# Kernel tuning notes

Hardware: AMD Instinct MI355X
Metric: run time of the kernel (lower is better)

The kernel has to match this reference:

```python
import jax, jax.numpy as jnp
import numpy as np

N = 50000      # nodes
E = 800000     # edges
IN = 128       # in_feats
HID = 16       # h_feats (per head)
HEADS = 8      # num_heads layer 1
CLS = 40       # num_classes
NEG_SLOPE = 0.2


def setup_inputs() -> dict:
    key = jax.random.key(0)
    ks = jax.random.split(key, 12)
    s = lambda fan: np.float32(1.0 / np.sqrt(fan))
    return {
        "features": jax.random.normal(ks[0], (N, IN), jnp.float32),
        "edge_src": jax.random.randint(ks[1], (E,), 0, N, dtype=jnp.int32),
        "edge_dst": jax.random.randint(ks[2], (E,), 0, N, dtype=jnp.int32),
        # layer 1 params
        "W1": jax.random.normal(ks[3], (IN, HEADS * HID), jnp.float32) * s(IN),
        "al1": jax.random.normal(ks[4], (HEADS, HID), jnp.float32) * s(HID),
        "ar1": jax.random.normal(ks[5], (HEADS, HID), jnp.float32) * s(HID),
        "b1": jnp.zeros((HEADS * HID,), jnp.float32),
        # layer 2 params (1 head)
        "W2": jax.random.normal(ks[6], (HEADS * HID, CLS), jnp.float32) * s(HEADS * HID),
        "al2": jax.random.normal(ks[7], (1, CLS), jnp.float32) * s(CLS),
        "ar2": jax.random.normal(ks[8], (1, CLS), jnp.float32) * s(CLS),
        "b2": jnp.zeros((CLS,), jnp.float32),
    }


def gat_conv(x, W, al, ar, b, src, dst, heads, out_dim):
    # x: [N, F_in] -> feat: [N, H, D]
    feat = (x @ W).reshape(-1, heads, out_dim)
    el = (feat * al).sum(-1)                      # [N, H]
    er = (feat * ar).sum(-1)                      # [N, H]
    e = jax.nn.leaky_relu(el[src] + er[dst], NEG_SLOPE)  # [E, H]
    # segment softmax over destination neighborhoods
    emax = jax.ops.segment_max(e, dst, num_segments=N)   # [N, H]
    emax = jnp.where(jnp.isfinite(emax), emax, jnp.float32(0.0))
    ee = jnp.exp(e - emax[dst])                   # [E, H]
    denom = jax.ops.segment_sum(ee, dst, num_segments=N)
    alpha = ee / (denom[dst] + jnp.float32(1e-9)) # [E, H]
    msg = alpha[:, :, None] * feat[src]           # [E, H, D]
    out = jax.ops.segment_sum(msg, dst, num_segments=N)  # [N, H, D]
    return out + b.reshape(1, heads, out_dim)


def reference(features, edge_src, edge_dst, W1, al1, ar1, b1, W2, al2, ar2, b2):
    h = jax.nn.elu(gat_conv(features, W1, al1, ar1, b1, edge_src, edge_dst, HEADS, HID))
    h = h.reshape(N, HEADS * HID)                 # flatten(1)
    out = gat_conv(h, W2, al2, ar2, b2, edge_src, edge_dst, 1, CLS)
    return out.mean(axis=1)                       # [N, CLS]
```

## Files before the change

### kernel.cpp

```cpp
#include <hip/hip_runtime.h>
#include <hip/hip_bf16.h>

#define N_NODES 50000
#define N_EDGES 800000
#define IN_F    128
#define HID     16
#define HEADS   8
#define F1      128
#define CLS     40
#define CLSP    64
#define NEG     0.2f
#define SLOT    64

#define SCAT_BLOCKS  ((N_EDGES + 255) / 256)

typedef __bf16 bf16x8 __attribute__((ext_vector_type(8)));
typedef float  f32x4  __attribute__((ext_vector_type(4)));
typedef float  f32x2  __attribute__((ext_vector_type(2)));

__device__ __forceinline__ float leaky(float v) { return v >= 0.0f ? v : NEG * v; }
__device__ __forceinline__ f32x2 unpk(unsigned u) {
    f32x2 r;
    r.x = __uint_as_float(u << 16);
    r.y = __uint_as_float(u & 0xffff0000u);
    return r;
}

__global__ void setup_kernel(const float* __restrict__ W1, const float* __restrict__ W2,
                             __bf16* __restrict__ w1t, __bf16* __restrict__ w2t,
                             int* __restrict__ cursor) {
    int i = blockIdx.x * blockDim.x + threadIdx.x;
    if (i < N_NODES) cursor[i] = 0;
    if (i < 128 * 128) {
        int n = i >> 7, k = i & 127;
        w1t[i] = (__bf16)W1[k * 128 + n];
    }
    if (i < CLSP * 128) {
        int n = i >> 7, k = i & 127;
        w2t[i] = (n < CLS) ? (__bf16)W2[k * CLS + n] : (__bf16)0.0f;
    }
}

__global__ __launch_bounds__(256) void scatter_kernel(const int* __restrict__ src,
                                                      const int* __restrict__ dst,
                                                      int* __restrict__ cursor,
                                                      unsigned short* __restrict__ srcs16) {
    int e = blockIdx.x * 256 + threadIdx.x;
    if (e >= N_EDGES) return;
    int d = dst[e];
    int c = atomicAdd(&cursor[d], 1);
    if (c < SLOT) srcs16[d * SLOT + c] = (unsigned short)src[e];
}

__global__ __launch_bounds__(256) void gemm1_mfma(const float* __restrict__ A,
                                                  const __bf16* __restrict__ Wt,
                                                  const float* __restrict__ al1,
                                                  const float* __restrict__ ar1,
                                                  __bf16* __restrict__ outb,
                                                  float* __restrict__ el,
                                                  float* __restrict__ er) {
    int wave = threadIdx.x >> 6, lane = threadIdx.x & 63;
    int m0 = blockIdx.x * 64 + wave * 16;
    int c = lane & 15;
    int row = m0 + c;
    int rowc = row < N_NODES ? row : N_NODES - 1;
    int ko = (lane >> 4) * 8;

    f32x4 acc[8];
    #pragma unroll
    for (int t = 0; t < 8; ++t)
        #pragma unroll
        for (int r = 0; r < 4; ++r) acc[t][r] = 0.f;

    for (int ks = 0; ks < 128; ks += 32) {
        const float* ap = A + (size_t)rowc * 128 + ks + ko;
        float4 u = *(const float4*)ap;
        float4 v = *(const float4*)(ap + 4);
        bf16x8 a;
        a[0] = (__bf16)u.x; a[1] = (__bf16)u.y; a[2] = (__bf16)u.z; a[3] = (__bf16)u.w;
        a[4] = (__bf16)v.x; a[5] = (__bf16)v.y; a[6] = (__bf16)v.z; a[7] = (__bf16)v.w;
        #pragma unroll
        for (int t = 0; t < 8; ++t) {
            bf16x8 b = *(const bf16x8*)(Wt + (size_t)(t * 16 + c) * 128 + ks + ko);
            acc[t] = __builtin_amdgcn_mfma_f32_16x16x32_bf16(a, b, acc[t], 0, 0, 0);
        }
    }
    int rbase = m0 + (lane >> 4) * 4;
    #pragma unroll
    for (int t = 0; t < 8; ++t) {
        int gcol = t * 16 + c;
        #pragma unroll
        for (int r = 0; r < 4; ++r) {
            int grow = rbase + r;
            if (grow < N_NODES) outb[(size_t)grow * 128 + gcol] = (__bf16)acc[t][r];
        }
    }
    #pragma unroll
    for (int t = 0; t < 8; ++t) {
        float alv = al1[t * 16 + c];
        float arv = ar1[t * 16 + c];
        float pe[4], pr[4];
        #pragma unroll
        for (int r = 0; r < 4; ++r) { pe[r] = acc[t][r] * alv; pr[r] = acc[t][r] * arv; }
        #pragma unroll
        for (int mask = 1; mask <= 8; mask <<= 1) {
            #pragma unroll
            for (int r = 0; r < 4; ++r) {
                pe[r] += __shfl_xor(pe[r], mask, 64);
                pr[r] += __shfl_xor(pr[r], mask, 64);
            }
        }
        if (c == 0) {
            #pragma unroll
            for (int r = 0; r < 4; ++r) {
                int grow = rbase + r;
                if (grow < N_NODES) {
                    el[grow * 8 + t] = pe[r];
                    er[grow * 8 + t] = pr[r];
                }
            }
        }
    }
}

__global__ __launch_bounds__(256) void gemm2_mfma(const __bf16* __restrict__ A,
                                                  const __bf16* __restrict__ Wt,
                                                  const float* __restrict__ al2,
                                                  const float* __restrict__ ar2,
                                                  __bf16* __restrict__ out,
                                                  float* __restrict__ el,
                                                  float* __restrict__ er) {
    int wave = threadIdx.x >> 6, lane = threadIdx.x & 63;
    int m0 = blockIdx.x * 64 + wave * 16;
    int c = lane & 15;
    int row = m0 + c;
    int rowc = row < N_NODES ? row : N_NODES - 1;
    int ko = (lane >> 4) * 8;

    f32x4 acc[4];
    #pragma unroll
    for (int t = 0; t < 4; ++t)
        #pragma unroll
        for (int r = 0; r < 4; ++r) acc[t][r] = 0.f;

    for (int ks = 0; ks < 128; ks += 32) {
        bf16x8 a = *(const bf16x8*)(A + (size_t)rowc * 128 + ks + ko);
        #pragma unroll
        for (int t = 0; t < 4; ++t) {
            bf16x8 b = *(const bf16x8*)(Wt + (size_t)(t * 16 + c) * 128 + ks + ko);
            acc[t] = __builtin_amdgcn_mfma_f32_16x16x32_bf16(a, b, acc[t], 0, 0, 0);
        }
    }
    int rbase = m0 + (lane >> 4) * 4;
    #pragma unroll
    for (int t = 0; t < 4; ++t) {
        int gcol = t * 16 + c;
        #pragma unroll
        for (int r = 0; r < 4; ++r) {
            int grow = rbase + r;
            if (grow < N_NODES) out[(size_t)grow * CLSP + gcol] = (__bf16)acc[t][r];
        }
    }
    float pe[4] = {0.f, 0.f, 0.f, 0.f}, pr[4] = {0.f, 0.f, 0.f, 0.f};
    #pragma unroll
    for (int t = 0; t < 3; ++t) {
        int idx = t * 16 + c;
        float alv = (idx < CLS) ? al2[idx] : 0.f;
        float arv = (idx < CLS) ? ar2[idx] : 0.f;
        #pragma unroll
        for (int r = 0; r < 4; ++r) { pe[r] += acc[t][r] * alv; pr[r] += acc[t][r] * arv; }
    }
    #pragma unroll
    for (int mask = 1; mask <= 8; mask <<= 1) {
        #pragma unroll
        for (int r = 0; r < 4; ++r) {
            pe[r] += __shfl_xor(pe[r], mask, 64);
            pr[r] += __shfl_xor(pr[r], mask, 64);
        }
    }
    if (c == 0) {
        #pragma unroll
        for (int r = 0; r < 4; ++r) {
            int grow = rbase + r;
            if (grow < N_NODES) { el[grow] = pe[r]; er[grow] = pr[r]; }
        }
    }
}

__global__ __launch_bounds__(256) void gat1_fused(const int* __restrict__ degs,
                                                  const unsigned short* __restrict__ srcs,
                                                  const float* __restrict__ el,
                                                  const float* __restrict__ er,
                                                  const __bf16* __restrict__ feat1b,
                                                  const float* __restrict__ b1,
                                                  __bf16* __restrict__ hbufb) {
    int wave = threadIdx.x >> 6;
    int lane = threadIdx.x & 63;
    int d = blockIdx.x * 4 + wave;
    int off = d * SLOT;
    int deg = min(degs[d], SLOT);

    int q = lane >> 4, fg = lane & 15, hd = fg >> 1;
    float er_d = er[d * 8 + hd];

    f32x2 accv[4];
    #pragma unroll
    for (int j = 0; j < 4; ++j) { accv[j].x = 0.f; accv[j].y = 0.f; }
    float dsum = 0.f;

    int ng = (deg + 3) >> 2;
    #pragma unroll 4
    for (int g = 0; g < ng; ++g) {
        int k = g * 4 + q;
        bool ok = k < deg;
        int s = ok ? (int)srcs[off + k] : 0;
        float elv = el[s * 8 + hd];
        uint4 p = *(const uint4*)(feat1b + (size_t)s * F1 + fg * 8);
        float w = ok ? __expf(leaky(elv + er_d)) : 0.f;
        dsum += w;
        f32x2 av; av.x = w; av.y = w;
        accv[0] += av * unpk(p.x);
        accv[1] += av * unpk(p.y);
        accv[2] += av * unpk(p.z);
        accv[3] += av * unpk(p.w);
    }

    float acc[8];
    #pragma unroll
    for (int j = 0; j < 4; ++j) { acc[2 * j] = accv[j].x; acc[2 * j + 1] = accv[j].y; }
    #pragma unroll
    for (int i = 0; i < 8; ++i) {
        acc[i] += __shfl_xor(acc[i], 16, 64);
        acc[i] += __shfl_xor(acc[i], 32, 64);
    }
    dsum += __shfl_xor(dsum, 16, 64);
    dsum += __shfl_xor(dsum, 32, 64);
    float inv_l = 1.f / (dsum + 1e-9f);

    if (q == 0) {
        bf16x8 o;
        #pragma unroll
        for (int i = 0; i < 8; ++i) {
            float v = acc[i] * inv_l + b1[fg * 8 + i];
            v = v > 0.f ? v : expm1f(v);
            o[i] = (__bf16)v;
        }
        *(bf16x8*)(hbufb + (size_t)d * F1 + fg * 8) = o;
    }
}

__global__ __launch_bounds__(256) void gat2_fused(const int* __restrict__ degs,
                                                  const unsigned short* __restrict__ srcs,
                                                  const float* __restrict__ el,
                                                  const float* __restrict__ er,
                                                  const __bf16* __restrict__ feat2p,
                                                  const float* __restrict__ b2,
                                                  float* __restrict__ out) {
    int wave = threadIdx.x >> 6;
    int lane = threadIdx.x & 63;
    int d = blockIdx.x * 4 + wave;
    int off = d * SLOT;
    int deg = min(degs[d], SLOT);

    float er_d = er[d];
    int q  = lane >> 4;
    int cg = lane & 15;
    f32x2 accv[2];
    accv[0].x = 0.f; accv[0].y = 0.f; accv[1].x = 0.f; accv[1].y = 0.f;
    float dsum = 0.f;

    int ng = (deg + 3) >> 2;
    #pragma unroll 4
    for (int g = 0; g < ng; ++g) {
        int k = g * 4 + q;
        bool ok = k < deg;
        int s = ok ? (int)srcs[off + k] : 0;
        float elv = el[s];
        uint2 p = *(const uint2*)(feat2p + (size_t)s * CLSP + cg * 4);
        float w = ok ? __expf(leaky(elv + er_d)) : 0.f;
        dsum += w;
        f32x2 av; av.x = w; av.y = w;
        accv[0] += av * unpk(p.x);
        accv[1] += av * unpk(p.y);
    }

    float acc[4];
    acc[0] = accv[0].x; acc[1] = accv[0].y; acc[2] = accv[1].x; acc[3] = accv[1].y;
    #pragma unroll
    for (int i = 0; i < 4; ++i) {
        acc[i] += __shfl_xor(acc[i], 16, 64);
        acc[i] += __shfl_xor(acc[i], 32, 64);
    }
    dsum += __shfl_xor(dsum, 16, 64);
    dsum += __shfl_xor(dsum, 32, 64);
    float inv_l = 1.f / (dsum + 1e-9f);

    if (lane < 10) {
        float4 o;
        o.x = acc[0] * inv_l + b2[cg * 4 + 0];
        o.y = acc[1] * inv_l + b2[cg * 4 + 1];
        o.z = acc[2] * inv_l + b2[cg * 4 + 2];
        o.w = acc[3] * inv_l + b2[cg * 4 + 3];
        *(float4*)(out + (size_t)d * CLS + cg * 4) = o;
    }
}

extern "C" void kernel_launch(void* const* d_in, const int* in_sizes, int n_in,
                              void* d_out, int out_size, void* d_ws, size_t ws_size,
                              hipStream_t stream) {
    const float* features = (const float*)d_in[0];
    const int*   esrc     = (const int*)d_in[1];
    const int*   edst     = (const int*)d_in[2];
    const float* W1       = (const float*)d_in[3];
    const float* al1      = (const float*)d_in[4];
    const float* ar1      = (const float*)d_in[5];
    const float* b1       = (const float*)d_in[6];
    const float* W2       = (const float*)d_in[7];
    const float* al2      = (const float*)d_in[8];
    const float* ar2      = (const float*)d_in[9];
    const float* b2       = (const float*)d_in[10];
    float* out = (float*)d_out;

    float* ws = (float*)d_ws;
    float*          el1    = ws;
    float*          er1    = ws + 400000;
    float*          el2    = ws + 800000;
    float*          er2    = ws + 850000;
    int*            cursor = (int*)(ws + 900000);
    unsigned short* srcs16 = (unsigned short*)(ws + 950000);
    __bf16*         feat1b = (__bf16*)(ws + 2550000);
    __bf16*         hbufb  = (__bf16*)(ws + 5750000);
    __bf16*         feat2p = (__bf16*)(ws + 8950000);
    __bf16*         w1t    = (__bf16*)(ws + 10550000);
    __bf16*         w2t    = (__bf16*)(ws + 10558192);

    const int B = 256;

    setup_kernel<<<(N_NODES + B - 1) / B, B, 0, stream>>>(W1, W2, w1t, w2t, cursor);

    scatter_kernel<<<SCAT_BLOCKS, B, 0, stream>>>(esrc, edst, cursor, srcs16);

    gemm1_mfma<<<(N_NODES + 63) / 64, B, 0, stream>>>(features, w1t, al1, ar1,
                                                      feat1b, el1, er1);

    gat1_fused<<<N_NODES / 4, B, 0, stream>>>(cursor, srcs16, el1, er1, feat1b, b1, hbufb);

    gemm2_mfma<<<(N_NODES + 63) / 64, B, 0, stream>>>(hbufb, w2t, al2, ar2,
                                                      feat2p, el2, er2);

    gat2_fused<<<N_NODES / 4, B, 0, stream>>>(cursor, srcs16, el2, er2, feat2p, b2, out);
}
```

Baseline: 273.6 us.

## Fuse scatter into gemm1 launch and fold layer-2 GEMM into gat1 epilogue

```diff
diff --git a/kernel.cpp b/kernel.cpp
--- a/kernel.cpp
+++ b/kernel.cpp
@@ -11,7 +11,10 @@
 #define CLSP    64
 #define NEG     0.2f
 #define SLOT    64
-
+#define SWEEPS      8
+#define SWEEP_RANGE 6250
+
+#define GEMM1_BLOCKS ((N_NODES + 63) / 64)
 #define SCAT_BLOCKS  ((N_EDGES + 255) / 256)
 
 typedef __bf16 bf16x8 __attribute__((ext_vector_type(8)));
@@ -41,26 +44,16 @@
     }
 }
 
-__global__ __launch_bounds__(256) void scatter_kernel(const int* __restrict__ src,
-                                                      const int* __restrict__ dst,
-                                                      int* __restrict__ cursor,
-                                                      unsigned short* __restrict__ srcs16) {
-    int e = blockIdx.x * 256 + threadIdx.x;
-    if (e >= N_EDGES) return;
-    int d = dst[e];
-    int c = atomicAdd(&cursor[d], 1);
-    if (c < SLOT) srcs16[d * SLOT + c] = (unsigned short)src[e];
-}
-
-__global__ __launch_bounds__(256) void gemm1_mfma(const float* __restrict__ A,
-                                                  const __bf16* __restrict__ Wt,
-                                                  const float* __restrict__ al1,
-                                                  const float* __restrict__ ar1,
-                                                  __bf16* __restrict__ outb,
-                                                  float* __restrict__ el,
-                                                  float* __restrict__ er) {
-    int wave = threadIdx.x >> 6, lane = threadIdx.x & 63;
-    int m0 = blockIdx.x * 64 + wave * 16;
+__device__ __forceinline__ void gemm1_body(int bid, int tid,
+                                           const float* __restrict__ A,
+                                           const __bf16* __restrict__ Wt,
+                                           const float* __restrict__ al1,
+                                           const float* __restrict__ ar1,
+                                           __bf16* __restrict__ outb,
+                                           float* __restrict__ el,
+                                           float* __restrict__ er) {
+    int wave = tid >> 6, lane = tid & 63;
+    int m0 = bid * 64 + wave * 16;
     int c = lane & 15;
     int row = m0 + c;
     int rowc = row < N_NODES ? row : N_NODES - 1;
@@ -123,68 +116,38 @@
     }
 }
 
-__global__ __launch_bounds__(256) void gemm2_mfma(const __bf16* __restrict__ A,
-                                                  const __bf16* __restrict__ Wt,
-                                                  const float* __restrict__ al2,
-                                                  const float* __restrict__ ar2,
-                                                  __bf16* __restrict__ out,
-                                                  float* __restrict__ el,
-                                                  float* __restrict__ er) {
-    int wave = threadIdx.x >> 6, lane = threadIdx.x & 63;
-    int m0 = blockIdx.x * 64 + wave * 16;
-    int c = lane & 15;
-    int row = m0 + c;
-    int rowc = row < N_NODES ? row : N_NODES - 1;
-    int ko = (lane >> 4) * 8;
-
-    f32x4 acc[4];
-    #pragma unroll
-    for (int t = 0; t < 4; ++t)
-        #pragma unroll
-        for (int r = 0; r < 4; ++r) acc[t][r] = 0.f;
-
-    for (int ks = 0; ks < 128; ks += 32) {
-        bf16x8 a = *(const bf16x8*)(A + (size_t)rowc * 128 + ks + ko);
-        #pragma unroll
-        for (int t = 0; t < 4; ++t) {
-            bf16x8 b = *(const bf16x8*)(Wt + (size_t)(t * 16 + c) * 128 + ks + ko);
-            acc[t] = __builtin_amdgcn_mfma_f32_16x16x32_bf16(a, b, acc[t], 0, 0, 0);
-        }
-    }
-    int rbase = m0 + (lane >> 4) * 4;
-    #pragma unroll
-    for (int t = 0; t < 4; ++t) {
-        int gcol = t * 16 + c;
-        #pragma unroll
-        for (int r = 0; r < 4; ++r) {
-            int grow = rbase + r;
-            if (grow < N_NODES) out[(size_t)grow * CLSP + gcol] = (__bf16)acc[t][r];
-        }
-    }
-    float pe[4] = {0.f, 0.f, 0.f, 0.f}, pr[4] = {0.f, 0.f, 0.f, 0.f};
-    #pragma unroll
-    for (int t = 0; t < 3; ++t) {
-        int idx = t * 16 + c;
-        float alv = (idx < CLS) ? al2[idx] : 0.f;
-        float arv = (idx < CLS) ? ar2[idx] : 0.f;
-        #pragma unroll
-        for (int r = 0; r < 4; ++r) { pe[r] += acc[t][r] * alv; pr[r] += acc[t][r] * arv; }
-    }
-    #pragma unroll
-    for (int mask = 1; mask <= 8; mask <<= 1) {
-        #pragma unroll
-        for (int r = 0; r < 4; ++r) {
-            pe[r] += __shfl_xor(pe[r], mask, 64);
-            pr[r] += __shfl_xor(pr[r], mask, 64);
-        }
-    }
-    if (c == 0) {
-        #pragma unroll
-        for (int r = 0; r < 4; ++r) {
-            int grow = rbase + r;
-            if (grow < N_NODES) { el[grow] = pe[r]; er[grow] = pr[r]; }
-        }
-    }
+__device__ __forceinline__ void scatter_body(int abs_bid, int rel_bid, int tid,
+                                             const int* __restrict__ src,
+                                             const int* __restrict__ dst,
+                                             int* __restrict__ cursor,
+                                             unsigned short* __restrict__ srcs16) {
+    int sweep = abs_bid & 7;
+    int chunk = rel_bid >> 3;
+    int e = chunk * 256 + tid;
+    if (e >= N_EDGES) return;
+    int d = dst[e];
+    int lo = sweep * SWEEP_RANGE;
+    if (d < lo || d >= lo + SWEEP_RANGE) return;
+    int c = atomicAdd(&cursor[d], 1);
+    if (c < SLOT) srcs16[d * SLOT + c] = (unsigned short)src[e];
+}
+
+__global__ __launch_bounds__(256) void fat_gemm1_scatter(const float* __restrict__ A,
+                                                         const __bf16* __restrict__ Wt,
+                                                         const float* __restrict__ al1,
+                                                         const float* __restrict__ ar1,
+                                                         __bf16* __restrict__ outb,
+                                                         float* __restrict__ el,
+                                                         float* __restrict__ er,
+                                                         const int* __restrict__ esrc,
+                                                         const int* __restrict__ edst,
+                                                         int* __restrict__ cursor,
+                                                         unsigned short* __restrict__ srcs16) {
+    if (blockIdx.x < GEMM1_BLOCKS)
+        gemm1_body(blockIdx.x, threadIdx.x, A, Wt, al1, ar1, outb, el, er);
+    else
+        scatter_body(blockIdx.x, blockIdx.x - GEMM1_BLOCKS, threadIdx.x,
+                     esrc, edst, cursor, srcs16);
 }
 
 __global__ __launch_bounds__(256) void gat1_fused(const int* __restrict__ degs,
@@ -193,7 +156,13 @@
                                                   const float* __restrict__ er,
                                                   const __bf16* __restrict__ feat1b,
                                                   const float* __restrict__ b1,
-                                                  __bf16* __restrict__ hbufb) {
+                                                  const __bf16* __restrict__ w2t,
+                                                  const float* __restrict__ al2,
+                                                  const float* __restrict__ ar2,
+                                                  float* __restrict__ el2,
+                                                  float* __restrict__ er2,
+                                                  __bf16* __restrict__ feat2p) {
+    __shared__ float h_lds[4][128];
     int wave = threadIdx.x >> 6;
     int lane = threadIdx.x & 63;
     int d = blockIdx.x * 4 + wave;
@@ -237,16 +206,45 @@
     dsum += __shfl_xor(dsum, 32, 64);
     float inv_l = 1.f / (dsum + 1e-9f);
 
+    float hv[8];
+    #pragma unroll
+    for (int i = 0; i < 8; ++i) {
+        float v = acc[i] * inv_l + b1[fg * 8 + i];
+        hv[i] = v > 0.f ? v : expm1f(v);
+    }
     if (q == 0) {
-        bf16x8 o;
-        #pragma unroll
-        for (int i = 0; i < 8; ++i) {
-            float v = acc[i] * inv_l + b1[fg * 8 + i];
-            v = v > 0.f ? v : expm1f(v);
-            o[i] = (__bf16)v;
-        }
-        *(bf16x8*)(hbufb + (size_t)d * F1 + fg * 8) = o;
-    }
+        f32x4 a0, a1;
+        a0[0] = hv[0]; a0[1] = hv[1]; a0[2] = hv[2]; a0[3] = hv[3];
+        a1[0] = hv[4]; a1[1] = hv[5]; a1[2] = hv[6]; a1[3] = hv[7];
+        *(f32x4*)&h_lds[wave][fg * 8]     = a0;
+        *(f32x4*)&h_lds[wave][fg * 8 + 4] = a1;
+    }
+    __syncthreads();
+
+    int c = lane;
+    const __bf16* w2row = w2t + (size_t)c * 128;
+    float f2 = 0.f;
+    #pragma unroll
+    for (int j0 = 0; j0 < 128; j0 += 8) {
+        f32x4 ha = *(const f32x4*)&h_lds[wave][j0];
+        f32x4 hb = *(const f32x4*)&h_lds[wave][j0 + 4];
+        bf16x8 wv = *(const bf16x8*)(w2row + j0);
+        f2 += ha[0] * (float)wv[0] + ha[1] * (float)wv[1]
+            + ha[2] * (float)wv[2] + ha[3] * (float)wv[3]
+            + hb[0] * (float)wv[4] + hb[1] * (float)wv[5]
+            + hb[2] * (float)wv[6] + hb[3] * (float)wv[7];
+    }
+
+    float a2v = (c < CLS) ? al2[c] : 0.f;
+    float r2v = (c < CLS) ? ar2[c] : 0.f;
+    float pe = f2 * a2v, pr = f2 * r2v;
+    #pragma unroll
+    for (int mask = 1; mask <= 32; mask <<= 1) {
+        pe += __shfl_xor(pe, mask, 64);
+        pr += __shfl_xor(pr, mask, 64);
+    }
+    if (lane == 0) { el2[d] = pe; er2[d] = pr; }
+    feat2p[(size_t)d * CLSP + c] = (__bf16)f2;
 }
 
 __global__ __launch_bounds__(256) void gat2_fused(const int* __restrict__ degs,
@@ -329,24 +327,19 @@
     int*            cursor = (int*)(ws + 900000);
     unsigned short* srcs16 = (unsigned short*)(ws + 950000);
     __bf16*         feat1b = (__bf16*)(ws + 2550000);
-    __bf16*         hbufb  = (__bf16*)(ws + 5750000);
-    __bf16*         feat2p = (__bf16*)(ws + 8950000);
-    __bf16*         w1t    = (__bf16*)(ws + 10550000);
-    __bf16*         w2t    = (__bf16*)(ws + 10558192);
+    __bf16*         feat2p = (__bf16*)(ws + 5750000);
+    __bf16*         w1t    = (__bf16*)(ws + 7350000);
+    __bf16*         w2t    = (__bf16*)(ws + 7358192);
 
     const int B = 256;
 
     setup_kernel<<<(N_NODES + B - 1) / B, B, 0, stream>>>(W1, W2, w1t, w2t, cursor);
 
-    scatter_kernel<<<SCAT_BLOCKS, B, 0, stream>>>(esrc, edst, cursor, srcs16);
-
-    gemm1_mfma<<<(N_NODES + 63) / 64, B, 0, stream>>>(features, w1t, al1, ar1,
-                                                      feat1b, el1, er1);
-
-    gat1_fused<<<N_NODES / 4, B, 0, stream>>>(cursor, srcs16, el1, er1, feat1b, b1, hbufb);
-
-    gemm2_mfma<<<(N_NODES + 63) / 64, B, 0, stream>>>(hbufb, w2t, al2, ar2,
-                                                      feat2p, el2, er2);
+    fat_gemm1_scatter<<<GEMM1_BLOCKS + SWEEPS * SCAT_BLOCKS, B, 0, stream>>>(
+        features, w1t, al1, ar1, feat1b, el1, er1, esrc, edst, cursor, srcs16);
+
+    gat1_fused<<<N_NODES / 4, B, 0, stream>>>(cursor, srcs16, el1, er1, feat1b, b1,
+                                              w2t, al2, ar2, el2, er2, feat2p);
 
     gat2_fused<<<N_NODES / 4, B, 0, stream>>>(cursor, srcs16, el2, er2, feat2p, b2, out);
 }
```

After: 422.1 us. 54.3% more time.

## Merge gemm1 and edge scatter into one launch; store feat2 unpadded

Applied to the files above, without the earlier changes.

```diff
diff --git a/kernel.cpp b/kernel.cpp
--- a/kernel.cpp
+++ b/kernel.cpp
@@ -12,6 +12,7 @@
 #define NEG     0.2f
 #define SLOT    64
 
+#define GEMM1_BLOCKS ((N_NODES + 63) / 64)
 #define SCAT_BLOCKS  ((N_EDGES + 255) / 256)
 
 typedef __bf16 bf16x8 __attribute__((ext_vector_type(8)));
@@ -41,26 +42,16 @@
     }
 }
 
-__global__ __launch_bounds__(256) void scatter_kernel(const int* __restrict__ src,
-                                                      const int* __restrict__ dst,
-                                                      int* __restrict__ cursor,
-                                                      unsigned short* __restrict__ srcs16) {
-    int e = blockIdx.x * 256 + threadIdx.x;
-    if (e >= N_EDGES) return;
-    int d = dst[e];
-    int c = atomicAdd(&cursor[d], 1);
-    if (c < SLOT) srcs16[d * SLOT + c] = (unsigned short)src[e];
-}
-
-__global__ __launch_bounds__(256) void gemm1_mfma(const float* __restrict__ A,
-                                                  const __bf16* __restrict__ Wt,
-                                                  const float* __restrict__ al1,
-                                                  const float* __restrict__ ar1,
-                                                  __bf16* __restrict__ outb,
-                                                  float* __restrict__ el,
-                                                  float* __restrict__ er) {
-    int wave = threadIdx.x >> 6, lane = threadIdx.x & 63;
-    int m0 = blockIdx.x * 64 + wave * 16;
+__device__ __forceinline__ void gemm1_body(int bid, int tid,
+                                           const float* __restrict__ A,
+                                           const __bf16* __restrict__ Wt,
+                                           const float* __restrict__ al1,
+                                           const float* __restrict__ ar1,
+                                           __bf16* __restrict__ outb,
+                                           float* __restrict__ el,
+                                           float* __restrict__ er) {
+    int wave = tid >> 6, lane = tid & 63;
+    int m0 = bid * 64 + wave * 16;
     int c = lane & 15;
     int row = m0 + c;
     int rowc = row < N_NODES ? row : N_NODES - 1;
@@ -121,6 +112,35 @@
             }
         }
     }
+}
+
+__device__ __forceinline__ void scatter_body(int bid, int tid,
+                                             const int* __restrict__ src,
+                                             const int* __restrict__ dst,
+                                             int* __restrict__ cursor,
+                                             unsigned short* __restrict__ srcs16) {
+    int e = bid * 256 + tid;
+    if (e >= N_EDGES) return;
+    int d = dst[e];
+    int c = atomicAdd(&cursor[d], 1);
+    if (c < SLOT) srcs16[d * SLOT + c] = (unsigned short)src[e];
+}
+
+__global__ __launch_bounds__(256) void fat_gemm1_scatter(const float* __restrict__ A,
+                                                         const __bf16* __restrict__ Wt,
+                                                         const float* __restrict__ al1,
+                                                         const float* __restrict__ ar1,
+                                                         __bf16* __restrict__ outb,
+                                                         float* __restrict__ el,
+                                                         float* __restrict__ er,
+                                                         const int* __restrict__ esrc,
+                                                         const int* __restrict__ edst,
+                                                         int* __restrict__ cursor,
+                                                         unsigned short* __restrict__ srcs16) {
+    if (blockIdx.x < GEMM1_BLOCKS)
+        gemm1_body(blockIdx.x, threadIdx.x, A, Wt, al1, ar1, outb, el, er);
+    else
+        scatter_body(blockIdx.x - GEMM1_BLOCKS, threadIdx.x, esrc, edst, cursor, srcs16);
 }
 
 __global__ __launch_bounds__(256) void gemm2_mfma(const __bf16* __restrict__ A,
@@ -137,28 +157,29 @@
     int rowc = row < N_NODES ? row : N_NODES - 1;
     int ko = (lane >> 4) * 8;
 
-    f32x4 acc[4];
-    #pragma unroll
-    for (int t = 0; t < 4; ++t)
+    f32x4 acc[3];
+    #pragma unroll
+    for (int t = 0; t < 3; ++t)
         #pragma unroll
         for (int r = 0; r < 4; ++r) acc[t][r] = 0.f;
 
     for (int ks = 0; ks < 128; ks += 32) {
         bf16x8 a = *(const bf16x8*)(A + (size_t)rowc * 128 + ks + ko);
         #pragma unroll
-        for (int t = 0; t < 4; ++t) {
+        for (int t = 0; t < 3; ++t) {
             bf16x8 b = *(const bf16x8*)(Wt + (size_t)(t * 16 + c) * 128 + ks + ko);
             acc[t] = __builtin_amdgcn_mfma_f32_16x16x32_bf16(a, b, acc[t], 0, 0, 0);
         }
     }
     int rbase = m0 + (lane >> 4) * 4;
     #pragma unroll
-    for (int t = 0; t < 4; ++t) {
+    for (int t = 0; t < 3; ++t) {
         int gcol = t * 16 + c;
         #pragma unroll
         for (int r = 0; r < 4; ++r) {
             int grow = rbase + r;
-            if (grow < N_NODES) out[(size_t)grow * CLSP + gcol] = (__bf16)acc[t][r];
+            if (grow < N_NODES && gcol < CLS)
+                out[(size_t)grow * CLS + gcol] = (__bf16)acc[t][r];
         }
     }
     float pe[4] = {0.f, 0.f, 0.f, 0.f}, pr[4] = {0.f, 0.f, 0.f, 0.f};
@@ -276,7 +297,9 @@
         bool ok = k < deg;
         int s = ok ? (int)srcs[off + k] : 0;
         float elv = el[s];
-        uint2 p = *(const uint2*)(feat2p + (size_t)s * CLSP + cg * 4);
+        uint2 p;
+        p.x = 0u; p.y = 0u;
+        if (cg < 10) p = *(const uint2*)(feat2p + (size_t)s * CLS + cg * 4);
         float w = ok ? __expf(leaky(elv + er_d)) : 0.f;
         dsum += w;
         f32x2 av; av.x = w; av.y = w;
@@ -331,17 +354,15 @@
     __bf16*         feat1b = (__bf16*)(ws + 2550000);
     __bf16*         hbufb  = (__bf16*)(ws + 5750000);
     __bf16*         feat2p = (__bf16*)(ws + 8950000);
-    __bf16*         w1t    = (__bf16*)(ws + 10550000);
-    __bf16*         w2t    = (__bf16*)(ws + 10558192);
+    __bf16*         w1t    = (__bf16*)(ws + 9950000);
+    __bf16*         w2t    = (__bf16*)(ws + 9958192);
 
     const int B = 256;
 
     setup_kernel<<<(N_NODES + B - 1) / B, B, 0, stream>>>(W1, W2, w1t, w2t, cursor);
 
-    scatter_kernel<<<SCAT_BLOCKS, B, 0, stream>>>(esrc, edst, cursor, srcs16);
-
-    gemm1_mfma<<<(N_NODES + 63) / 64, B, 0, stream>>>(features, w1t, al1, ar1,
-                                                      feat1b, el1, er1);
+    fat_gemm1_scatter<<<GEMM1_BLOCKS + SCAT_BLOCKS, B, 0, stream>>>(
+        features, w1t, al1, ar1, feat1b, el1, er1, esrc, edst, cursor, srcs16);
 
     gat1_fused<<<N_NODES / 4, B, 0, stream>>>(cursor, srcs16, el1, er1, feat1b, b1, hbufb);
 
```

New measurement: 239.4 us. -12.5%, faster.
